# Performance work log

Hardware: AMD Instinct MI355X
Metric: run time of the kernel (lower is better)

## Reference

```python
import jax, jax.numpy as jnp
import numpy as np

N_NODES = 50000
N_EDGES = 800000
N_REL = 2
K_SEL = 4096


def _glorot(key, shape):
    fan = shape[-2] + shape[-1]
    lim = jnp.sqrt(6.0 / fan)
    return jax.random.uniform(key, shape, minval=-lim, maxval=lim, dtype=jnp.float32)


def setup_inputs() -> dict:
    key = jax.random.key(0)
    ks = jax.random.split(key, 12)
    x = jax.random.normal(ks[0], (N_NODES, 128), jnp.float32)
    edge_index = jax.random.randint(ks[1], (2, N_EDGES), 0, N_NODES)
    edge_type = jax.random.randint(ks[2], (N_EDGES,), 0, N_REL)
    idx = jax.random.randint(ks[3], (K_SEL,), 0, N_NODES)
    # RGATConv 0: in=128, out=128, heads=2, dim=1 -> concat width 256
    w0 = _glorot(ks[4], (N_REL, 128, 256))
    q0 = _glorot(ks[5], (256, 2))
    k0 = _glorot(ks[6], (256, 2))
    b0 = jnp.zeros((256,), jnp.float32)
    g0 = jnp.ones((256,), jnp.float32)
    be0 = jnp.zeros((256,), jnp.float32)
    # RGATConv 1: in=256, out=128, heads=1
    w1 = _glorot(ks[7], (N_REL, 256, 128))
    q1 = _glorot(ks[8], (128, 1))
    k1 = _glorot(ks[9], (128, 1))
    b1 = jnp.zeros((128,), jnp.float32)
    g1 = jnp.ones((128,), jnp.float32)
    be1 = jnp.zeros((128,), jnp.float32)
    wm = _glorot(ks[10], (128, 5))
    bm = jnp.zeros((5,), jnp.float32)
    return dict(x=x, edge_index=edge_index, edge_type=edge_type, idx=idx,
                w0=w0, q0=q0, k0=k0, b0=b0, g0=g0, be0=be0,
                w1=w1, q1=q1, k1=k1, b1=b1, g1=g1, be1=be1, wm=wm, bm=bm)


def _segment_softmax(a, index, num_segments):
    # PyG utils.softmax: per-target max-shifted exp, normalized with +1e-16
    m = jax.ops.segment_max(a, index, num_segments=num_segments)
    m = jnp.where(jnp.isfinite(m), m, 0.0)
    e = jnp.exp(a - m[index])
    s = jax.ops.segment_sum(e, index, num_segments=num_segments)
    return e / (s[index] + 1e-16)


def _rgat(x, W, q, k, b, src, dst, edge_type, heads, out_ch, n):
    # additive-self-attention, across-relation, dim=1, aggr='add' (PyG defaults)
    xw = jnp.einsum('ni,rio->rno', x, W)          # [R, N, H*O]
    out_i = xw[edge_type, dst]                    # [E, H*O] gathered per edge
    out_j = xw[edge_type, src]                    # [E, H*O]
    alpha = jax.nn.leaky_relu(out_i @ q + out_j @ k, 0.2)   # [E, H]
    alpha = _segment_softmax(alpha, dst, n)
    msg = (alpha[:, :, None] * out_j.reshape(-1, heads, out_ch)).reshape(-1, heads * out_ch)
    return jax.ops.segment_sum(msg, dst, num_segments=n) + b


def _bn(h, g, b):
    # training-mode BatchNorm over nodes (biased var, eps=1e-5)
    mu = jnp.mean(h, axis=0)
    var = jnp.var(h, axis=0)
    return g * (h - mu) * jax.lax.rsqrt(var + 1e-5) + b


def reference(x, edge_index, edge_type, idx, w0, q0, k0, b0, g0, be0,
              w1, q1, k1, b1, g1, be1, wm, bm):
    n = x.shape[0]
    src, dst = edge_index[0], edge_index[1]
    h = jax.nn.leaky_relu(_rgat(x, w0, q0, k0, b0, src, dst, edge_type, 2, 128, n), 0.01)
    h = _bn(h, g0, be0)
    h = jax.nn.leaky_relu(_rgat(h, w1, q1, k1, b1, src, dst, edge_type, 1, 128, n), 0.01)
    h = _bn(h, g1, be1)
    h = h[idx]                                   # index_select over nodes
    out = jax.nn.sigmoid(h @ wm + bm)
    return (h, out)
```

## Files before the change

kernel.cpp:

```cpp
#include <hip/hip_runtime.h>
#include <hip/hip_bf16.h>
#include <math.h>


#define WAVE 64

typedef short     s16x8 __attribute__((ext_vector_type(8)));
typedef ushort    u16x8 __attribute__((ext_vector_type(8)));
typedef float     f32x4 __attribute__((ext_vector_type(4)));
typedef _Float16  f16x8 __attribute__((ext_vector_type(8)));

__device__ inline ushort bf_rne(float x) {
  uint u = __float_as_uint(x);
  return (ushort)((u + 0x7FFFu + ((u >> 16) & 1u)) >> 16);
}
__device__ inline ushort bf_hi_resid(float x, float& resid) {
  uint u = __float_as_uint(x);
  uint r = (u + 0x7FFFu + ((u >> 16) & 1u)) & 0xFFFF0000u;
  resid = x - __uint_as_float(r);
  return (ushort)(r >> 16);
}
__device__ inline float bf2f(ushort h) {
  return __uint_as_float(((uint)h) << 16);
}

__global__ __launch_bounds__(256) void k_hist(const int* __restrict__ dst,
                                              int* __restrict__ deg, int E) {
  int e = blockIdx.x * blockDim.x + threadIdx.x;
  if (e < E) atomicAdd(&deg[dst[e]], 1);
}

__global__ __launch_bounds__(256) void k_scan_blk(const int* __restrict__ deg,
                                                  int* __restrict__ bsum, int n) {
  int i = blockIdx.x * 256 + threadIdx.x;
  int v = (i < n) ? deg[i] : 0;
#pragma unroll
  for (int o = 32; o; o >>= 1) v += __shfl_xor(v, o);
  __shared__ int ws[4];
  if ((threadIdx.x & 63) == 0) ws[threadIdx.x >> 6] = v;
  __syncthreads();
  if (threadIdx.x == 0) bsum[blockIdx.x] = ws[0] + ws[1] + ws[2] + ws[3];
}

__global__ __launch_bounds__(256) void k_scan_top(int* __restrict__ bsum, int nb,
                                                  int* __restrict__ rowptr_n,
                                                  int E) {
  __shared__ int sh[256];
  int t = threadIdx.x;
  int carry = 0;
  for (int base = 0; base < nb; base += 256) {
    int i = base + t;
    int v = (i < nb) ? bsum[i] : 0;
    sh[t] = v;
    __syncthreads();
    for (int o = 1; o < 256; o <<= 1) {
      int u = (t >= o) ? sh[t - o] : 0;
      __syncthreads();
      sh[t] += u;
      __syncthreads();
    }
    if (i < nb) bsum[i] = carry + sh[t] - v;
    int blockTotal = sh[255];
    __syncthreads();
    carry += blockTotal;
  }
  if (t == 0) *rowptr_n = E;
}

__global__ __launch_bounds__(256) void k_scan_fin(const int* __restrict__ deg,
                                                  const int* __restrict__ bsum,
                                                  int* __restrict__ rowptr,
                                                  int* __restrict__ cursor, int n) {
  int t = threadIdx.x;
  int i = blockIdx.x * 256 + t;
  int v = (i < n) ? deg[i] : 0;
  __shared__ int sh[256];
  sh[t] = v;
  __syncthreads();
  for (int o = 1; o < 256; o <<= 1) {
    int u = (t >= o) ? sh[t - o] : 0;
    __syncthreads();
    sh[t] += u;
    __syncthreads();
  }
  if (i < n) {
    int ex = bsum[blockIdx.x] + sh[t] - v;
    rowptr[i] = ex;
    cursor[i] = ex;
  }
}

__global__ __launch_bounds__(256) void k_scatter(const int* __restrict__ dst,
                                                 int* __restrict__ cursor,
                                                 int* __restrict__ csr, int E) {
  int e = blockIdx.x * blockDim.x + threadIdx.x;
  if (e < E) {
    int p = atomicAdd(&cursor[dst[e]], 1);
    csr[p] = e;
  }
}

__global__ __launch_bounds__(256) void k_split(const float* __restrict__ in,
                                               ushort* __restrict__ hi,
                                               ushort* __restrict__ lo, int n4) {
  int i = blockIdx.x * blockDim.x + threadIdx.x;
  if (i >= n4) return;
  float4 v = ((const float4*)in)[i];
  float r0, r1, r2, r3;
  ushort4 hv, lv;
  hv.x = bf_hi_resid(v.x, r0); lv.x = bf_rne(r0);
  hv.y = bf_hi_resid(v.y, r1); lv.y = bf_rne(r1);
  hv.z = bf_hi_resid(v.z, r2); lv.z = bf_rne(r2);
  hv.w = bf_hi_resid(v.w, r3); lv.w = bf_rne(r3);
  ((ushort4*)hi)[i] = hv;
  ((ushort4*)lo)[i] = lv;
}

__global__ __launch_bounds__(256) void k_convW(const float* __restrict__ w,
                                               ushort* __restrict__ thi,
                                               ushort* __restrict__ tlo,
                                               const float* __restrict__ scale,
                                               int R, int K, int N) {
  int i = blockIdx.x * blockDim.x + threadIdx.x;
  if (i >= R * K * N) return;
  int n  = i % N;
  int t  = i / N;
  int kk = t % K;
  int r  = t / K;
  float x = w[i];
  if (scale) x *= scale[kk];
  float resid;
  ushort h = bf_hi_resid(x, resid);
  size_t o = ((size_t)r * N + n) * K + kk;
  thi[o] = h;
  tlo[o] = bf_rne(resid);
}

__global__ __launch_bounds__(256) void k_biasW(const float* __restrict__ w,
                                               const float* __restrict__ shf,
                                               float* __restrict__ cbias,
                                               int R, int K, int N) {
  int t = blockIdx.x * blockDim.x + threadIdx.x;
  if (t >= R * N) return;
  int n = t % N, r = t / N;
  float s = 0.f;
  for (int k = 0; k < K; ++k)
    s += shf[k] * w[((size_t)r * K + k) * N + n];
  cbias[t] = s;
}

__global__ __launch_bounds__(256) void k_gemm_mfma(
    const ushort* __restrict__ Ahi, const ushort* __restrict__ Alo,
    const ushort* __restrict__ Bhi, const ushort* __restrict__ Blo,
    const float* __restrict__ cbias, _Float16* __restrict__ C,
    int M, int K, int N) {
  const int r  = blockIdx.z;
  const int n0 = blockIdx.x * 128;
  const int m0 = blockIdx.y * 128;
  __shared__ __align__(16) ushort Ah[128][40];
  __shared__ __align__(16) ushort Al[128][40];
  __shared__ __align__(16) ushort Bh[128][40];
  __shared__ __align__(16) ushort Bl[128][40];
  const int tid  = threadIdx.x;
  const int lane = tid & 63;
  const int wid  = tid >> 6;
  const int wr = wid >> 1, wc = wid & 1;
  const int lr = lane & 15;
  const int lk = (lane >> 4) * 8;
  const size_t bbase = (size_t)r * N * K;

  f32x4 acc[4][4];
#pragma unroll
  for (int i = 0; i < 4; ++i)
#pragma unroll
    for (int j = 0; j < 4; ++j) acc[i][j] = (f32x4){0.f, 0.f, 0.f, 0.f};

  for (int k0 = 0; k0 < K; k0 += 32) {
#pragma unroll
    for (int rep = 0; rep < 2; ++rep) {
      int idx = tid + rep * 256;
      int row = idx >> 2, piece = idx & 3;
      int gm = m0 + row;
      s16x8 vh = (s16x8)0, vl = (s16x8)0;
      if (gm < M) {
        size_t ga = (size_t)gm * K + k0 + piece * 8;
        vh = *(const s16x8*)(Ahi + ga);
        vl = *(const s16x8*)(Alo + ga);
      }
      *(s16x8*)&Ah[row][piece * 8] = vh;
      *(s16x8*)&Al[row][piece * 8] = vl;
    }
#pragma unroll
    for (int rep = 0; rep < 2; ++rep) {
      int idx = tid + rep * 256;
      int col = idx >> 2, piece = idx & 3;
      size_t ga = bbase + (size_t)(n0 + col) * K + k0 + piece * 8;
      *(s16x8*)&Bh[col][piece * 8] = *(const s16x8*)(Bhi + ga);
      *(s16x8*)&Bl[col][piece * 8] = *(const s16x8*)(Blo + ga);
    }
    __syncthreads();

    s16x8 ah[4], al[4], bh[4], bl[4];
#pragma unroll
    for (int f = 0; f < 4; ++f) {
      ah[f] = *(const s16x8*)&Ah[wr * 64 + f * 16 + lr][lk];
      al[f] = *(const s16x8*)&Al[wr * 64 + f * 16 + lr][lk];
      bh[f] = *(const s16x8*)&Bh[wc * 64 + f * 16 + lr][lk];
      bl[f] = *(const s16x8*)&Bl[wc * 64 + f * 16 + lr][lk];
    }
#pragma unroll
    for (int fi = 0; fi < 4; ++fi)
#pragma unroll
      for (int fj = 0; fj < 4; ++fj) {
        acc[fi][fj] = __builtin_amdgcn_mfma_f32_16x16x32_bf16(
            ah[fi], bh[fj], acc[fi][fj], 0, 0, 0);
        acc[fi][fj] = __builtin_amdgcn_mfma_f32_16x16x32_bf16(
            ah[fi], bl[fj], acc[fi][fj], 0, 0, 0);
        acc[fi][fj] = __builtin_amdgcn_mfma_f32_16x16x32_bf16(
            al[fi], bh[fj], acc[fi][fj], 0, 0, 0);
      }
    __syncthreads();
  }

  float bz[4] = {0.f, 0.f, 0.f, 0.f};
  if (cbias) {
#pragma unroll
    for (int fj = 0; fj < 4; ++fj)
      bz[fj] = cbias[r * N + n0 + wc * 64 + fj * 16 + lr];
  }
  _Float16* Cr = C + (size_t)r * M * N;
#pragma unroll
  for (int fi = 0; fi < 4; ++fi) {
#pragma unroll
    for (int v = 0; v < 4; ++v) {
      int row = m0 + wr * 64 + fi * 16 + (lane >> 4) * 4 + v;
      if (row < M) {
        size_t rb = (size_t)row * N + n0 + wc * 64 + lr;
#pragma unroll
        for (int fj = 0; fj < 4; ++fj)
          Cr[rb + fj * 16] = (_Float16)(acc[fi][fj][v] + bz[fj]);
      }
    }
  }
}

template <int C, int H>
__global__ __launch_bounds__(256) void k_logits(const _Float16* __restrict__ xw,
                                                const float* __restrict__ qm,
                                                const float* __restrict__ km,
                                                float* __restrict__ ai,
                                                float* __restrict__ aj,
                                                int totalRows) {
  int g = blockIdx.x * blockDim.x + threadIdx.x;
  int row = g >> 2, q4 = g & 3;
  if (row >= totalRows) return;
  constexpr int QC = C / 4;
  const _Float16* rp = xw + (size_t)row * C + q4 * QC;
  float pq[H] = {}, pk[H] = {};
  for (int b = 0; b < QC; b += 8) {
    f16x8 v = *(const f16x8*)(rp + b);
#pragma unroll
    for (int e = 0; e < 8; ++e) {
      float f = (float)v[e];
      int c = q4 * QC + b + e;
#pragma unroll
      for (int h = 0; h < H; ++h) {
        pq[h] += f * qm[c * H + h];
        pk[h] += f * km[c * H + h];
      }
    }
  }
#pragma unroll
  for (int h = 0; h < H; ++h) {
    pq[h] += __shfl_xor(pq[h], 1); pq[h] += __shfl_xor(pq[h], 2);
    pk[h] += __shfl_xor(pk[h], 1); pk[h] += __shfl_xor(pk[h], 2);
  }
  if (q4 == 0) {
#pragma unroll
    for (int h = 0; h < H; ++h) {
      ai[(size_t)row * H + h] = pq[h];
      aj[(size_t)row * H + h] = pk[h];
    }
  }
}

template <int C, int H, bool SPLIT>
__global__ __launch_bounds__(256) void k_agg(const int* __restrict__ rowptr,
                                             const int* __restrict__ csr,
                                             const int* __restrict__ srcIdx,
                                             const int* __restrict__ etype,
                                             const float* __restrict__ ai,
                                             const float* __restrict__ aj,
                                             const _Float16* __restrict__ xw,
                                             const float* __restrict__ bias,
                                             float* __restrict__ out32,
                                             ushort* __restrict__ ohi,
                                             ushort* __restrict__ olo,
                                             int nNodes) {
  constexpr int LPE = C / 8;
  constexpr int EPW = WAVE / LPE;
  constexpr int OC  = C / H;
  int wid  = (blockIdx.x * blockDim.x + threadIdx.x) >> 6;
  int lane = threadIdx.x & 63;
  if (wid >= nNodes) return;
  const int node  = wid;
  const int start = rowptr[node];
  const int end   = rowptr[node + 1];
  const int deg   = end - start;

  float aiv[2][H];
#pragma unroll
  for (int rr = 0; rr < 2; ++rr)
#pragma unroll
    for (int h = 0; h < H; ++h)
      aiv[rr][h] = ai[((size_t)rr * nNodes + node) * H + h];

  if (deg <= WAVE) {
    int i = start + lane;
    bool valid = i < end;
    int e = valid ? csr[i] : 0;
    int s = valid ? srcIdx[e] : 0;
    int t = valid ? etype[e] : 0;
    float a[H], eh[H], m[H], ssum[H];
#pragma unroll
    for (int h = 0; h < H; ++h) {
      float v = aiv[t][h] + aj[((size_t)t * nNodes + s) * H + h];
      v = v > 0.f ? v : 0.2f * v;
      a[h] = valid ? v : -1e30f;
      m[h] = a[h];
    }
#pragma unroll
    for (int h = 0; h < H; ++h)
#pragma unroll
      for (int o = 32; o; o >>= 1) m[h] = fmaxf(m[h], __shfl_xor(m[h], o));
#pragma unroll
    for (int h = 0; h < H; ++h) {
      eh[h] = valid ? expf(a[h] - m[h]) : 0.f;
      ssum[h] = eh[h];
#pragma unroll
      for (int o = 32; o; o >>= 1) ssum[h] += __shfl_xor(ssum[h], o);
    }

    const int sub = lane / LPE;
    const int cl  = lane % LPE;
    const int c0  = cl * 8;
    const int myhead = c0 / OC;

    float acc[8] = {};
#pragma unroll 2
    for (int j = 0; j < deg; j += EPW) {
      int je = j + sub;
      int   sj = __shfl(s, je);
      int   tj = __shfl(t, je);
      float cc0 = __shfl(eh[0], je);
      float coef;
      if (H == 1) coef = cc0;
      else { float cc1 = __shfl(eh[H - 1], je); coef = myhead ? cc1 : cc0; }
      f16x8 rv = *(const f16x8*)(xw + ((size_t)tj * nNodes + sj) * C + c0);
#pragma unroll
      for (int v = 0; v < 8; ++v) acc[v] += coef * (float)rv[v];
    }
#pragma unroll
    for (int v = 0; v < 8; ++v) {
      if (EPW == 4) acc[v] += __shfl_xor(acc[v], 16);
      acc[v] += __shfl_xor(acc[v], 32);
    }
    float inv = 1.f / (ssum[myhead] + 1e-16f);
    if (sub == 0) {
      if constexpr (SPLIT) {
        u16x8 hv, lv;
#pragma unroll
        for (int v = 0; v < 8; ++v) {
          float xo = acc[v] * inv + bias[c0 + v];
          xo = xo > 0.f ? xo : 0.01f * xo;
          float resid;
          hv[v] = bf_hi_resid(xo, resid);
          lv[v] = bf_rne(resid);
        }
        *(u16x8*)&ohi[(size_t)node * C + c0] = hv;
        *(u16x8*)&olo[(size_t)node * C + c0] = lv;
      } else {
        float ov[8];
#pragma unroll
        for (int v = 0; v < 8; ++v) {
          float xo = acc[v] * inv + bias[c0 + v];
          ov[v] = xo > 0.f ? xo : 0.01f * xo;
        }
        *(float4*)&out32[(size_t)node * C + c0]     = *(float4*)&ov[0];
        *(float4*)&out32[(size_t)node * C + c0 + 4] = *(float4*)&ov[4];
      }
    }
  } else {
    constexpr int VEC = C / WAVE;
    const int myhead = (lane * VEC) / OC;
    float acc[VEC] = {};
    float ssum[H] = {};
    float m[H];
#pragma unroll
    for (int h = 0; h < H; ++h) m[h] = -1e30f;
    for (int i = start + lane; i < end; i += WAVE) {
      int e = csr[i];
      int s = srcIdx[e];
      int t = etype[e];
#pragma unroll
      for (int h = 0; h < H; ++h) {
        float v = aiv[t][h] + aj[((size_t)t * nNodes + s) * H + h];
        v = v > 0.f ? v : 0.2f * v;
        m[h] = fmaxf(m[h], v);
      }
    }
#pragma unroll
    for (int h = 0; h < H; ++h)
#pragma unroll
      for (int o = 32; o; o >>= 1) m[h] = fmaxf(m[h], __shfl_xor(m[h], o));
    for (int base = start; base < end; base += WAVE) {
      int i = base + lane;
      bool valid = i < end;
      int e = valid ? csr[i] : 0;
      int s = valid ? srcIdx[e] : 0;
      int t = valid ? etype[e] : 0;
      float eh[H];
#pragma unroll
      for (int h = 0; h < H; ++h) {
        float v = aiv[t][h] + aj[((size_t)t * nNodes + s) * H + h];
        v = v > 0.f ? v : 0.2f * v;
        eh[h] = valid ? expf(v - m[h]) : 0.f;
        ssum[h] += eh[h];
      }
      int cnt = end - base; if (cnt > WAVE) cnt = WAVE;
#pragma unroll 4
      for (int j = 0; j < cnt; ++j) {
        int   sj = __shfl(s, j);
        int   tj = __shfl(t, j);
        float cc0 = __shfl(eh[0], j);
        float coef;
        if (H == 1) coef = cc0;
        else { float cc1 = __shfl(eh[H - 1], j); coef = myhead ? cc1 : cc0; }
        const _Float16* row = xw + ((size_t)tj * nNodes + sj) * C + lane * VEC;
#pragma unroll
        for (int v = 0; v < VEC; ++v) acc[v] += coef * (float)row[v];
      }
    }
#pragma unroll
    for (int h = 0; h < H; ++h)
#pragma unroll
      for (int o = 32; o; o >>= 1) ssum[h] += __shfl_xor(ssum[h], o);
    float inv = 1.f / (ssum[myhead] + 1e-16f);
#pragma unroll
    for (int v = 0; v < VEC; ++v) {
      int c = lane * VEC + v;
      float xo = acc[v] * inv + bias[c];
      xo = xo > 0.f ? xo : 0.01f * xo;
      if constexpr (SPLIT) {
        float resid;
        ohi[(size_t)node * C + c] = bf_hi_resid(xo, resid);
        olo[(size_t)node * C + c] = bf_rne(resid);
      } else {
        out32[(size_t)node * C + c] = xo;
      }
    }
  }
}

__global__ void k_bn_stats(const float* __restrict__ h, double* __restrict__ sum,
                           double* __restrict__ sumsq, int nNodes, int C) {
  int col = threadIdx.x;
  int r0 = blockIdx.x * 256;
  int r1 = r0 + 256; if (r1 > nNodes) r1 = nNodes;
  float s = 0.f, s2 = 0.f;
  for (int r = r0; r < r1; ++r) {
    float v = h[(size_t)r * C + col];
    s += v;
    s2 = fmaf(v, v, s2);
  }
  atomicAdd(&sum[col], (double)s);
  atomicAdd(&sumsq[col], (double)s2);
}

__global__ void k_bn_stats_hl(const ushort* __restrict__ hi,
                              const ushort* __restrict__ lo,
                              double* __restrict__ sum,
                              double* __restrict__ sumsq, int nNodes, int C) {
  int col = threadIdx.x;
  int r0 = blockIdx.x * 256;
  int r1 = r0 + 256; if (r1 > nNodes) r1 = nNodes;
  float s = 0.f, s2 = 0.f;
  for (int r = r0; r < r1; ++r) {
    size_t o = (size_t)r * C + col;
    float v = bf2f(hi[o]) + bf2f(lo[o]);
    s += v;
    s2 = fmaf(v, v, s2);
  }
  atomicAdd(&sum[col], (double)s);
  atomicAdd(&sumsq[col], (double)s2);
}

__global__ void k_bn_finalize(const double* __restrict__ sum,
                              const double* __restrict__ sumsq,
                              const float* __restrict__ g,
                              const float* __restrict__ be,
                              float* __restrict__ scale,
                              float* __restrict__ shift, int nNodes, int C) {
  int c = blockIdx.x * blockDim.x + threadIdx.x;
  if (c >= C) return;
  double mu  = sum[c] / nNodes;
  double var = sumsq[c] / nNodes - mu * mu;
  float rs = (float)(1.0 / sqrt(var + 1e-5));
  float sc = g[c] * rs;
  scale[c] = sc;
  shift[c] = be[c] - (float)mu * sc;
}

__global__ __launch_bounds__(256) void k_head(const float* __restrict__ h,
                                              const int* __restrict__ idx,
                                              const float* __restrict__ scl,
                                              const float* __restrict__ shf,
                                              const float* __restrict__ wm,
                                              const float* __restrict__ bm,
                                              float* __restrict__ outH,
                                              float* __restrict__ outP, int kSel) {
  int wid  = (blockIdx.x * blockDim.x + threadIdx.x) >> 6;
  int lane = threadIdx.x & 63;
  if (wid >= kSel) return;
  int node = idx[wid];
  const float* row = h + (size_t)node * 128;
  int c = lane * 2;
  float2 v = *(const float2*)&row[c];
  v.x = v.x * scl[c + 0] + shf[c + 0];
  v.y = v.y * scl[c + 1] + shf[c + 1];
  *(float2*)&outH[(size_t)wid * 128 + c] = v;
  float p0 = v.x * wm[c * 5 + 0] + v.y * wm[(c + 1) * 5 + 0];
  float p1 = v.x * wm[c * 5 + 1] + v.y * wm[(c + 1) * 5 + 1];
  float p2 = v.x * wm[c * 5 + 2] + v.y * wm[(c + 1) * 5 + 2];
  float p3 = v.x * wm[c * 5 + 3] + v.y * wm[(c + 1) * 5 + 3];
  float p4 = v.x * wm[c * 5 + 4] + v.y * wm[(c + 1) * 5 + 4];
#pragma unroll
  for (int o = 32; o; o >>= 1) {
    p0 += __shfl_xor(p0, o); p1 += __shfl_xor(p1, o); p2 += __shfl_xor(p2, o);
    p3 += __shfl_xor(p3, o); p4 += __shfl_xor(p4, o);
  }
  if (lane == 0) {
    float lg[5] = {p0 + bm[0], p1 + bm[1], p2 + bm[2], p3 + bm[3], p4 + bm[4]};
    float* o = &outP[(size_t)wid * 5];
    o[0] = 1.f / (1.f + expf(-lg[0]));
    o[1] = 1.f / (1.f + expf(-lg[1]));
    o[2] = 1.f / (1.f + expf(-lg[2]));
    o[3] = 1.f / (1.f + expf(-lg[3]));
    o[4] = 1.f / (1.f + expf(-lg[4]));
  }
}

extern "C" void kernel_launch(void* const* d_in, const int* in_sizes, int n_in,
                              void* d_out, int out_size, void* d_ws, size_t ws_size,
                              hipStream_t stream) {
  const float* x    = (const float*)d_in[0];
  const int*   ei   = (const int*)d_in[1];
  const int*   etyp = (const int*)d_in[2];
  const int*   idx  = (const int*)d_in[3];
  const float* w0   = (const float*)d_in[4];
  const float* q0   = (const float*)d_in[5];
  const float* k0   = (const float*)d_in[6];
  const float* b0   = (const float*)d_in[7];
  const float* g0   = (const float*)d_in[8];
  const float* be0  = (const float*)d_in[9];
  const float* w1   = (const float*)d_in[10];
  const float* q1   = (const float*)d_in[11];
  const float* k1   = (const float*)d_in[12];
  const float* b1   = (const float*)d_in[13];
  const float* g1   = (const float*)d_in[14];
  const float* be1  = (const float*)d_in[15];
  const float* wm   = (const float*)d_in[16];
  const float* bm   = (const float*)d_in[17];

  const int N    = in_sizes[0] / 128;
  const int E    = in_sizes[1] / 2;
  const int kSel = in_sizes[3];
  const int* srcIdx = ei;
  const int* dstIdx = ei + E;

  size_t off = 0;
  auto carve = [&](size_t bytes) -> void* {
    off = (off + 255) & ~(size_t)255;
    void* p = (char*)d_ws + off;
    off += bytes;
    return p;
  };
  int*      deg    = (int*)carve((size_t)N * 4);
  int*      rowptr = (int*)carve((size_t)(N + 1) * 4);
  int*      cursor = (int*)carve((size_t)N * 4);
  int*      bsum   = (int*)carve((size_t)((N + 255) / 256) * 4);
  int*      csr    = (int*)carve((size_t)E * 4);
  _Float16* xwh    = (_Float16*)carve((size_t)2 * N * 256 * 2);
  ushort*   Ahi    = (ushort*)carve((size_t)N * 256 * 2);
  ushort*   Alo    = (ushort*)carve((size_t)N * 256 * 2);
  ushort*   W0thi  = (ushort*)carve((size_t)2 * 256 * 128 * 2);
  ushort*   W0tlo  = (ushort*)carve((size_t)2 * 256 * 128 * 2);
  ushort*   W1thi  = (ushort*)carve((size_t)2 * 256 * 128 * 2);
  ushort*   W1tlo  = (ushort*)carve((size_t)2 * 256 * 128 * 2);
  float*    cbias1 = (float*)carve(256 * 4);
  float*    ai     = (float*)carve((size_t)2 * N * 2 * 4);
  float*    aj     = (float*)carve((size_t)2 * N * 2 * 4);
  float*    h1     = (float*)carve((size_t)N * 128 * 4);
  double*   dsum   = (double*)carve(256 * 8);
  double*   dsumsq = (double*)carve(256 * 8);
  float*    scl    = (float*)carve(256 * 4);
  float*    shf    = (float*)carve(256 * 4);

  float* outH = (float*)d_out;
  float* outP = outH + (size_t)kSel * 128;

  const int eb = (E + 255) / 256;
  const int nbBlocks = (N + 255) / 256;

  hipMemsetAsync(deg, 0, (size_t)N * 4, stream);
  k_hist<<<eb, 256, 0, stream>>>(dstIdx, deg, E);
  k_scan_blk<<<nbBlocks, 256, 0, stream>>>(deg, bsum, N);
  k_scan_top<<<1, 256, 0, stream>>>(bsum, nbBlocks, rowptr + N, E);
  k_scan_fin<<<nbBlocks, 256, 0, stream>>>(deg, bsum, rowptr, cursor, N);
  k_scatter<<<eb, 256, 0, stream>>>(dstIdx, cursor, csr, E);

  k_convW<<<(2 * 128 * 256 + 255) / 256, 256, 0, stream>>>(
      w0, W0thi, W0tlo, nullptr, 2, 128, 256);
  k_split<<<((N * 128 / 4) + 255) / 256, 256, 0, stream>>>(
      x, Ahi, Alo, N * 128 / 4);

  {
    dim3 grid(256 / 128, (N + 127) / 128, 2);
    k_gemm_mfma<<<grid, 256, 0, stream>>>(Ahi, Alo, W0thi, W0tlo, nullptr,
                                          xwh, N, 128, 256);
  }
  k_logits<256, 2><<<(2 * N * 4 + 255) / 256, 256, 0, stream>>>(
      xwh, q0, k0, ai, aj, 2 * N);
  k_agg<256, 2, true><<<(N * WAVE + 255) / 256, 256, 0, stream>>>(
      rowptr, csr, srcIdx, etyp, ai, aj, xwh, b0, nullptr, Ahi, Alo, N);
  hipMemsetAsync(dsum, 0, 256 * 8, stream);
  hipMemsetAsync(dsumsq, 0, 256 * 8, stream);
  k_bn_stats_hl<<<nbBlocks, 256, 0, stream>>>(Ahi, Alo, dsum, dsumsq, N, 256);
  k_bn_finalize<<<1, 256, 0, stream>>>(dsum, dsumsq, g0, be0, scl, shf, N, 256);

  k_convW<<<(2 * 256 * 128 + 255) / 256, 256, 0, stream>>>(
      w1, W1thi, W1tlo, scl, 2, 256, 128);
  k_biasW<<<1, 256, 0, stream>>>(w1, shf, cbias1, 2, 256, 128);

  {
    dim3 grid(128 / 128, (N + 127) / 128, 2);
    k_gemm_mfma<<<grid, 256, 0, stream>>>(Ahi, Alo, W1thi, W1tlo, cbias1,
                                          xwh, N, 256, 128);
  }
  k_logits<128, 1><<<(2 * N * 4 + 255) / 256, 256, 0, stream>>>(
      xwh, q1, k1, ai, aj, 2 * N);
  k_agg<128, 1, false><<<(N * WAVE + 255) / 256, 256, 0, stream>>>(
      rowptr, csr, srcIdx, etyp, ai, aj, xwh, b1, h1, nullptr, nullptr, N);
  hipMemsetAsync(dsum, 0, 128 * 8, stream);
  hipMemsetAsync(dsumsq, 0, 128 * 8, stream);
  k_bn_stats<<<nbBlocks, 128, 0, stream>>>(h1, dsum, dsumsq, N, 128);
  k_bn_finalize<<<1, 128, 0, stream>>>(dsum, dsumsq, g1, be1, scl, shf, N, 128);

  k_head<<<(kSel * WAVE + 255) / 256, 256, 0, stream>>>(
      h1, idx, scl, shf, wm, bm, outH, outP, kSel);
}
```

Measured before the change: 716.8 us.

## Fuse fp32 input split into GEMM, swizzle blocks across XCDs, parallelize biasW

Removes the standalone k_split kernel: the first GEMM now loads fp32 x directly and does the bf16 hi/lo split while staging tiles into shared memory. The GEMM block index is remapped so consecutive tiles land on the same XCD, which should improve L2 reuse of B and A. k_biasW switches from one thread per output to one wavefront per output with a shuffle reduction, and the aggregation loop's unroll factor goes from 2 to 4. The fused split repeats conversion work per N-tile and widens the A loads to fp32.

New measurement: 651.3 us. 9.1% less time.

```diff
diff --git a/kernel.cpp b/kernel.cpp
--- a/kernel.cpp
+++ b/kernel.cpp
@@ -98,22 +98,6 @@
     int p = atomicAdd(&cursor[dst[e]], 1);
     csr[p] = e;
   }
-}
-
-__global__ __launch_bounds__(256) void k_split(const float* __restrict__ in,
-                                               ushort* __restrict__ hi,
-                                               ushort* __restrict__ lo, int n4) {
-  int i = blockIdx.x * blockDim.x + threadIdx.x;
-  if (i >= n4) return;
-  float4 v = ((const float4*)in)[i];
-  float r0, r1, r2, r3;
-  ushort4 hv, lv;
-  hv.x = bf_hi_resid(v.x, r0); lv.x = bf_rne(r0);
-  hv.y = bf_hi_resid(v.y, r1); lv.y = bf_rne(r1);
-  hv.z = bf_hi_resid(v.z, r2); lv.z = bf_rne(r2);
-  hv.w = bf_hi_resid(v.w, r3); lv.w = bf_rne(r3);
-  ((ushort4*)hi)[i] = hv;
-  ((ushort4*)lo)[i] = lv;
 }
 
 __global__ __launch_bounds__(256) void k_convW(const float* __restrict__ w,
@@ -140,23 +124,37 @@
                                                const float* __restrict__ shf,
                                                float* __restrict__ cbias,
                                                int R, int K, int N) {
-  int t = blockIdx.x * blockDim.x + threadIdx.x;
-  if (t >= R * N) return;
-  int n = t % N, r = t / N;
+  int wid  = (blockIdx.x * blockDim.x + threadIdx.x) >> 6;
+  int lane = threadIdx.x & 63;
+  if (wid >= R * N) return;
+  int n = wid % N, r = wid / N;
   float s = 0.f;
-  for (int k = 0; k < K; ++k)
+  for (int k = lane; k < K; k += WAVE)
     s += shf[k] * w[((size_t)r * K + k) * N + n];
-  cbias[t] = s;
-}
-
+#pragma unroll
+  for (int o = 32; o; o >>= 1) s += __shfl_xor(s, o);
+  if (lane == 0) cbias[wid] = s;
+}
+
+template <bool A32>
 __global__ __launch_bounds__(256) void k_gemm_mfma(
-    const ushort* __restrict__ Ahi, const ushort* __restrict__ Alo,
-    const ushort* __restrict__ Bhi, const ushort* __restrict__ Blo,
-    const float* __restrict__ cbias, _Float16* __restrict__ C,
-    int M, int K, int N) {
-  const int r  = blockIdx.z;
-  const int n0 = blockIdx.x * 128;
-  const int m0 = blockIdx.y * 128;
+    const float* __restrict__ A, const ushort* __restrict__ Ahi,
+    const ushort* __restrict__ Alo, const ushort* __restrict__ Bhi,
+    const ushort* __restrict__ Blo, const float* __restrict__ cbias,
+    _Float16* __restrict__ C, int M, int K, int N) {
+  const int nwgx = gridDim.x, nwgy = gridDim.y;
+  int nwg = nwgx * nwgy * gridDim.z;
+  int lin = blockIdx.x + nwgx * (blockIdx.y + nwgy * blockIdx.z);
+  int q = nwg >> 3, rmd = nwg & 7, xcd = lin & 7, pos = lin >> 3;
+  int swz = (xcd < rmd) ? xcd * (q + 1) + pos
+                        : rmd * (q + 1) + (xcd - rmd) * q + pos;
+  const int bx = swz % nwgx;
+  const int by = (swz / nwgx) % nwgy;
+  const int bz = swz / (nwgx * nwgy);
+
+  const int r  = bz;
+  const int n0 = bx * 128;
+  const int m0 = by * 128;
   __shared__ __align__(16) ushort Ah[128][40];
   __shared__ __align__(16) ushort Al[128][40];
   __shared__ __align__(16) ushort Bh[128][40];
@@ -181,14 +179,32 @@
       int idx = tid + rep * 256;
       int row = idx >> 2, piece = idx & 3;
       int gm = m0 + row;
-      s16x8 vh = (s16x8)0, vl = (s16x8)0;
-      if (gm < M) {
-        size_t ga = (size_t)gm * K + k0 + piece * 8;
-        vh = *(const s16x8*)(Ahi + ga);
-        vl = *(const s16x8*)(Alo + ga);
-      }
-      *(s16x8*)&Ah[row][piece * 8] = vh;
-      *(s16x8*)&Al[row][piece * 8] = vl;
+      if constexpr (A32) {
+        f32x4 v0 = (f32x4){0.f, 0.f, 0.f, 0.f}, v1 = v0;
+        if (gm < M) {
+          const float* ga = A + (size_t)gm * K + k0 + piece * 8;
+          v0 = *(const f32x4*)ga;
+          v1 = *(const f32x4*)(ga + 4);
+        }
+        u16x8 hv, lv;
+        float resid;
+#pragma unroll
+        for (int e = 0; e < 4; ++e) {
+          hv[e] = bf_hi_resid(v0[e], resid); lv[e] = bf_rne(resid);
+          hv[e + 4] = bf_hi_resid(v1[e], resid); lv[e + 4] = bf_rne(resid);
+        }
+        *(u16x8*)&Ah[row][piece * 8] = hv;
+        *(u16x8*)&Al[row][piece * 8] = lv;
+      } else {
+        s16x8 vh = (s16x8)0, vl = (s16x8)0;
+        if (gm < M) {
+          size_t ga = (size_t)gm * K + k0 + piece * 8;
+          vh = *(const s16x8*)(Ahi + ga);
+          vl = *(const s16x8*)(Alo + ga);
+        }
+        *(s16x8*)&Ah[row][piece * 8] = vh;
+        *(s16x8*)&Al[row][piece * 8] = vl;
+      }
     }
 #pragma unroll
     for (int rep = 0; rep < 2; ++rep) {
@@ -222,11 +238,11 @@
     __syncthreads();
   }
 
-  float bz[4] = {0.f, 0.f, 0.f, 0.f};
+  float bz4[4] = {0.f, 0.f, 0.f, 0.f};
   if (cbias) {
 #pragma unroll
     for (int fj = 0; fj < 4; ++fj)
-      bz[fj] = cbias[r * N + n0 + wc * 64 + fj * 16 + lr];
+      bz4[fj] = cbias[r * N + n0 + wc * 64 + fj * 16 + lr];
   }
   _Float16* Cr = C + (size_t)r * M * N;
 #pragma unroll
@@ -238,7 +254,7 @@
         size_t rb = (size_t)row * N + n0 + wc * 64 + lr;
 #pragma unroll
         for (int fj = 0; fj < 4; ++fj)
-          Cr[rb + fj * 16] = (_Float16)(acc[fi][fj][v] + bz[fj]);
+          Cr[rb + fj * 16] = (_Float16)(acc[fi][fj][v] + bz4[fj]);
       }
     }
   }
@@ -347,7 +363,7 @@
     const int myhead = c0 / OC;
 
     float acc[8] = {};
-#pragma unroll 2
+#pragma unroll 4
     for (int j = 0; j < deg; j += EPW) {
       int je = j + sub;
       int   sj = __shfl(s, je);
@@ -621,13 +637,11 @@
 
   k_convW<<<(2 * 128 * 256 + 255) / 256, 256, 0, stream>>>(
       w0, W0thi, W0tlo, nullptr, 2, 128, 256);
-  k_split<<<((N * 128 / 4) + 255) / 256, 256, 0, stream>>>(
-      x, Ahi, Alo, N * 128 / 4);
 
   {
     dim3 grid(256 / 128, (N + 127) / 128, 2);
-    k_gemm_mfma<<<grid, 256, 0, stream>>>(Ahi, Alo, W0thi, W0tlo, nullptr,
-                                          xwh, N, 128, 256);
+    k_gemm_mfma<true><<<grid, 256, 0, stream>>>(
+        x, nullptr, nullptr, W0thi, W0tlo, nullptr, xwh, N, 128, 256);
   }
   k_logits<256, 2><<<(2 * N * 4 + 255) / 256, 256, 0, stream>>>(
       xwh, q0, k0, ai, aj, 2 * N);
@@ -640,12 +654,13 @@
 
   k_convW<<<(2 * 256 * 128 + 255) / 256, 256, 0, stream>>>(
       w1, W1thi, W1tlo, scl, 2, 256, 128);
-  k_biasW<<<1, 256, 0, stream>>>(w1, shf, cbias1, 2, 256, 128);
+  k_biasW<<<(2 * 128 * WAVE + 255) / 256, 256, 0, stream>>>(
+      w1, shf, cbias1, 2, 256, 128);
 
   {
     dim3 grid(128 / 128, (N + 127) / 128, 2);
-    k_gemm_mfma<<<grid, 256, 0, stream>>>(Ahi, Alo, W1thi, W1tlo, cbias1,
-                                          xwh, N, 256, 128);
+    k_gemm_mfma<false><<<grid, 256, 0, stream>>>(
+        nullptr, Ahi, Alo, W1thi, W1tlo, cbias1, xwh, N, 256, 128);
   }
   k_logits<128, 1><<<(2 * N * 4 + 255) / 256, 256, 0, stream>>>(
       xwh, q1, k1, ai, aj, 2 * N);
```
